# Kernel optimization log

Measured on AMD Instinct MI355X. Metric: run time of the kernel, lower is better.

Reference implementation:

```python
import jax, jax.numpy as jnp
import numpy as np

B, S, E, H, MLP = 2, 2048, 1024, 16, 4096
VEC = 8          # args.vec_length: block-row height of vector-sparse mask
SPARSITY = 0.9   # fraction of attention entries dropped
D = E // H


def _make_mask():
    # static_random_mask_aligned: each block-row of VEC query rows keeps a
    # random ~(1-sparsity) subset of key columns. Diagonal kept so every
    # softmax row is non-empty.
    rng = np.random.default_rng(0)
    block = rng.random((S // VEC, S)) < (1.0 - SPARSITY)   # [m, n]
    mask = np.repeat(block, VEC, axis=0)                   # [S, S]
    mask |= np.eye(S, dtype=bool)
    return jnp.asarray(mask)


def setup_inputs() -> dict:
    key = jax.random.key(0)
    ks = jax.random.split(key, 8)
    w = lambda k, shp: (0.02 * jax.random.normal(k, shp, dtype=jnp.float32))
    return {
        "x": jax.random.normal(ks[0], (B, S, E), dtype=jnp.float32),
        "mask": _make_mask(),                       # [S,S] bool, static
        "w_qkv": w(ks[1], (3 * E, E)),             # in_proj_weight
        "b_qkv": jnp.zeros((3 * E,), jnp.float32),
        "w_out": w(ks[2], (E, E)),                 # out_proj
        "b_out": jnp.zeros((E,), jnp.float32),
        "g1": jnp.ones((E,), jnp.float32), "beta1": jnp.zeros((E,), jnp.float32),
        "g2": jnp.ones((E,), jnp.float32), "beta2": jnp.zeros((E,), jnp.float32),
        "w1": w(ks[3], (MLP, E)), "bias1": jnp.zeros((MLP,), jnp.float32),
        "w2": w(ks[4], (E, MLP)), "bias2": jnp.zeros((E,), jnp.float32),
    }


def _layer_norm(x, g, b, eps=1e-5):
    mu = jnp.mean(x, axis=-1, keepdims=True)
    var = jnp.mean(jnp.square(x - mu), axis=-1, keepdims=True)
    return (x - mu) * jax.lax.rsqrt(var + eps) * g + b


def _sparse_mha(h, mask, w_qkv, b_qkv, w_out, b_out):
    qkv = jnp.einsum("bse,fe->bsf", h, w_qkv) + b_qkv       # [B,S,3E]
    q, k, v = jnp.split(qkv, 3, axis=-1)
    q = q.reshape(B, S, H, D)
    k = k.reshape(B, S, H, D)
    v = v.reshape(B, S, H, D)
    scores = jnp.einsum("bqhd,bkhd->bhqk", q, k) / jnp.sqrt(jnp.float32(D))
    scores = jnp.where(mask[None, None], scores, jnp.float32(-1e9))
    p = jax.nn.softmax(scores, axis=-1)
    ctx = jnp.einsum("bhqk,bkhd->bqhd", p, v).reshape(B, S, E)
    return jnp.einsum("bse,fe->bsf", ctx, w_out) + b_out


def reference(x, mask, w_qkv, b_qkv, w_out, b_out, g1, beta1, g2, beta2,
              w1, bias1, w2, bias2):
    h = _layer_norm(x, g1, beta1)
    attn = _sparse_mha(h, mask, w_qkv, b_qkv, w_out, b_out)
    out = attn + x                      # residual 1
    out = _layer_norm(out, g2, beta2)
    out = jnp.einsum("bse,me->bsm", out, w1) + bias1   # linear1 (no activation, as in source)
    out = jnp.einsum("bsm,em->bse", out, w2) + bias2   # linear2
    return out + x                      # residual adds ORIGINAL x (as in source)
```

## Files before the change

### kernel.cpp

```cpp
#include <hip/hip_runtime.h>
#include <cstdint>
#include <cstddef>

typedef unsigned short u16;
typedef unsigned int u32;
typedef short s16x8 __attribute__((ext_vector_type(8)));
typedef float f32x4 __attribute__((ext_vector_type(4)));
typedef _Float16 f16x2 __attribute__((ext_vector_type(2)));

__device__ __forceinline__ float fdot2(f16x2 a, f16x2 b, float c) {
#if defined(__HIP_DEVICE_COMPILE__) && __has_builtin(__builtin_amdgcn_fdot2)
  return __builtin_amdgcn_fdot2(a, b, c, false);
#else
  return (float)a.x * (float)b.x + (float)a.y * (float)b.y + c;
#endif
}

__device__ __forceinline__ float red8(float x) {
#if defined(__HIP_DEVICE_COMPILE__)
  asm("v_add_f32_dpp %0, %0, %0 quad_perm:[1,0,3,2] row_mask:0xf bank_mask:0xf"
      : "+v"(x));
  asm("v_add_f32_dpp %0, %0, %0 quad_perm:[2,3,0,1] row_mask:0xf bank_mask:0xf"
      : "+v"(x));
  asm("v_add_f32_dpp %0, %0, %0 row_half_mirror row_mask:0xf bank_mask:0xf"
      : "+v"(x));
  return x;
#else
  x += __shfl_xor(x, 1); x += __shfl_xor(x, 2); x += __shfl_xor(x, 4);
  return x;
#endif
}

__device__ __forceinline__ void fmamix_lo(float& a, u32 hv, float p) {
#if defined(__HIP_DEVICE_COMPILE__)
  asm("v_fma_mix_f32 %0, %1, %2, %0 op_sel_hi:[1,0,0]"
      : "+v"(a) : "v"(hv), "v"(p));
#else
  union { u32 i; _Float16 h[2]; } c; c.i = hv; a += (float)c.h[0] * p;
#endif
}
__device__ __forceinline__ void fmamix_hi(float& a, u32 hv, float p) {
#if defined(__HIP_DEVICE_COMPILE__)
  asm("v_fma_mix_f32 %0, %1, %2, %0 op_sel:[1,0,0] op_sel_hi:[1,0,0]"
      : "+v"(a) : "v"(hv), "v"(p));
#else
  union { u32 i; _Float16 h[2]; } c; c.i = hv; a += (float)c.h[1] * p;
#endif
}

#define S_LEN 2048
#define EMB   1024
#define NHEAD 16
#define HD    64
#define E3    3072
#define MLPD  4096
#define NROWS 4096
#define LCAP  640

__device__ __forceinline__ float bf2f(u16 v) {
  union { u32 i; float f; } c; c.i = ((u32)v) << 16; return c.f;
}
__device__ __forceinline__ u16 f2bf(float f) {
  union { float f; u32 i; } c; c.f = f;
  u32 x = c.i;
  return (u16)((x + 0x7FFFu + ((x >> 16) & 1u)) >> 16);
}
__device__ __forceinline__ u16 f2h(float f) {
  _Float16 h = (_Float16)f;
  union { _Float16 h; u16 b; } c; c.h = h; return c.b;
}

__device__ __forceinline__ void gl2lds16(const void* g, void* l) {
  __builtin_amdgcn_global_load_lds(
      (__attribute__((address_space(1))) void*)(g),
      (__attribute__((address_space(3))) void*)(l), 16, 0, 0);
}

__global__ void detect_flags(const u32* __restrict__ w1s, int* __restrict__ dtflag,
                             const u32* __restrict__ mask, int* __restrict__ maskrep) {
  __shared__ int hits[256];
  __shared__ u32 red[256];
  int h = 0; u32 v = 0;
  for (int i = threadIdx.x; i < 4096; i += 256) {
    u32 w = w1s[i];
    if ((w & 0xFFFFu) && (((w >> 7) & 0xFFu) >= 0xC8u)) ++h;
    v |= mask[i];
  }
  hits[threadIdx.x] = h; red[threadIdx.x] = v;
  __syncthreads();
  if (threadIdx.x == 0) {
    int t = 0; u32 o = 0;
    for (int i = 0; i < 256; ++i) { t += hits[i]; o |= red[i]; }
    *dtflag = (t > 8) ? 1 : 0;
    int rep;
    if (o <= 1u) rep = 0;
    else if (o & 0x80u) rep = 1;
    else if (o & 0x00800000u) rep = 2;
    else rep = 3;
    *maskrep = rep;
  }
}

__device__ __forceinline__ bool maskbit(const void* m, int rep, size_t idx) {
  switch (rep) {
    case 0:  return ((const int*)m)[idx] != 0;
    case 1:  return ((const u16*)m)[idx] != 0;
    case 2:  return ((const u32*)m)[idx] != 0;
    default: return ((const unsigned char*)m)[idx] != 0;
  }
}

__global__ __launch_bounds__(256)
void cvt_kernel(const void* __restrict__ src, u16* __restrict__ dst,
                int n8, const int* __restrict__ dtflag) {
  const int i = blockIdx.x * blockDim.x + threadIdx.x;
  if (i >= n8) return;
  if (*dtflag) {
    const float4 a = ((const float4*)src)[i * 2];
    const float4 b = ((const float4*)src)[i * 2 + 1];
    u16 o[8] = {f2bf(a.x), f2bf(a.y), f2bf(a.z), f2bf(a.w),
                f2bf(b.x), f2bf(b.y), f2bf(b.z), f2bf(b.w)};
    *(uint4*)(dst + (size_t)i * 8) = *(const uint4*)o;
  } else {
    ((uint4*)dst)[i] = ((const uint4*)src)[i];
  }
}

__global__ void cvt_small(const void* s0, u16* d0, const void* s1, u16* d1,
                          const void* s2, u16* d2, const void* s3, u16* d3,
                          const void* s4, u16* d4, const void* s5, u16* d5,
                          const void* s6, u16* d6, const void* s7, u16* d7,
                          const int* __restrict__ dtflag) {
  const int f = *dtflag;
  const void* srcs[8] = {s0, s1, s2, s3, s4, s5, s6, s7};
  u16* dsts[8] = {d0, d1, d2, d3, d4, d5, d6, d7};
  const int ns[8] = {E3, EMB, EMB, EMB, EMB, EMB, MLPD, EMB};
#pragma unroll
  for (int k = 0; k < 8; ++k) {
    for (int idx = threadIdx.x; idx < ns[k]; idx += 256)
      dsts[k][idx] = f ? f2bf(((const float*)srcs[k])[idx])
                       : ((const u16*)srcs[k])[idx];
  }
}

__global__ void build_lists(const void* __restrict__ mask, const int* __restrict__ repf,
                            int* __restrict__ lists, int* __restrict__ cnt,
                            unsigned char* __restrict__ diagflag) {
  __shared__ int num;
  const int m = blockIdx.x;
  if (threadIdx.x == 0) num = 0;
  __syncthreads();
  const int rep = *repf;
  const int row0 = m * 8;
  for (int j = threadIdx.x; j < S_LEN; j += 256) {
    int srcrow = (j == row0) ? (row0 + 1) : row0;
    bool bit = maskbit(mask, rep, (size_t)srcrow * S_LEN + j);
    if (j >= row0 && j < row0 + 8) diagflag[j] = bit ? 0 : 1;
    if (bit) {
      int p = atomicAdd(&num, 1);
      if (p < LCAP) lists[m * LCAP + p] = j * 4096;
    }
  }
  __syncthreads();
  if (threadIdx.x == 0) cnt[m] = (num < LCAP) ? num : LCAP;
}

__global__ __launch_bounds__(256)
void ln_kernel(const void* __restrict__ Xv, const u16* __restrict__ g,
               const u16* __restrict__ be, u16* __restrict__ O,
               const int* __restrict__ inf32) {
  const int wv = threadIdx.x >> 6, ln = threadIdx.x & 63;
  const int row = blockIdx.x * 4 + wv;
  float v[16];
  if (inf32 && *inf32) {
    const float* xr = (const float*)Xv + (size_t)row * EMB;
    float4 a0 = *(const float4*)(xr + ln * 8);
    float4 a1 = *(const float4*)(xr + ln * 8 + 4);
    float4 b0 = *(const float4*)(xr + 512 + ln * 8);
    float4 b1 = *(const float4*)(xr + 512 + ln * 8 + 4);
    v[0]=a0.x; v[1]=a0.y; v[2]=a0.z; v[3]=a0.w; v[4]=a1.x; v[5]=a1.y; v[6]=a1.z; v[7]=a1.w;
    v[8]=b0.x; v[9]=b0.y; v[10]=b0.z; v[11]=b0.w; v[12]=b1.x; v[13]=b1.y; v[14]=b1.z; v[15]=b1.w;
  } else {
    const u16* xr = (const u16*)Xv + (size_t)row * EMB;
    union { uint4 u; u16 s[8]; } p0, p1;
    p0.u = *(const uint4*)(xr + ln * 8);
    p1.u = *(const uint4*)(xr + 512 + ln * 8);
#pragma unroll
    for (int t = 0; t < 8; ++t) { v[t] = bf2f(p0.s[t]); v[8 + t] = bf2f(p1.s[t]); }
  }
  float s = 0.f, sq = 0.f;
#pragma unroll
  for (int t = 0; t < 16; ++t) { s += v[t]; sq += v[t] * v[t]; }
#pragma unroll
  for (int off = 32; off; off >>= 1) { s += __shfl_xor(s, off); sq += __shfl_xor(sq, off); }
  const float mu = s * (1.0f / EMB);
  const float var = sq * (1.0f / EMB) - mu * mu;
  const float rsig = rsqrtf(var + 1e-5f);
  union { uint4 u; u16 s[8]; } g0, g1v, b0, b1v, o0, o1;
  g0.u = *(const uint4*)(g + ln * 8);   g1v.u = *(const uint4*)(g + 512 + ln * 8);
  b0.u = *(const uint4*)(be + ln * 8);  b1v.u = *(const uint4*)(be + 512 + ln * 8);
#pragma unroll
  for (int t = 0; t < 8; ++t) {
    o0.s[t] = f2bf((v[t]     - mu) * rsig * bf2f(g0.s[t])  + bf2f(b0.s[t]));
    o1.s[t] = f2bf((v[8 + t] - mu) * rsig * bf2f(g1v.s[t]) + bf2f(b1v.s[t]));
  }
  u16* orow = O + (size_t)row * EMB;
  *(uint4*)(orow + ln * 8) = o0.u;
  *(uint4*)(orow + 512 + ln * 8) = o1.u;
}

__global__ __launch_bounds__(256)
void gemm_bt(const u16* __restrict__ A, const u16* __restrict__ B,
             const u16* __restrict__ bias, u16* __restrict__ C,
             int M, int N, int K) {
  __shared__ u16 a_sh[128 * 64];
  __shared__ u16 b_sh[128 * 64];
  const int tid = threadIdx.x;
  const int wv = tid >> 6, ln = tid & 63;
  const int wm = wv & 1, wn = wv >> 1;
  const int tm = blockIdx.y, tn = blockIdx.x;
  const int srow = ln >> 3;
  const int scol = ((ln & 7) ^ srow) * 8;
  const int q = ln >> 4, rr = ln & 15;

  f32x4 acc[4][4] = {};
  const u16* Abase = A + (size_t)(tm * 128) * K;
  const u16* Bbase = B + (size_t)(tn * 128) * K;

  for (int k0 = 0; k0 < K; k0 += 64) {
    __syncthreads();
#pragma unroll
    for (int c = 0; c < 4; ++c) {
      const int chunk = wv * 4 + c;
      const int row = chunk * 8 + srow;
      gl2lds16(Abase + (size_t)row * K + k0 + scol, &a_sh[chunk * 512]);
      gl2lds16(Bbase + (size_t)row * K + k0 + scol, &b_sh[chunk * 512]);
    }
    __syncthreads();
#pragma unroll
    for (int kk = 0; kk < 2; ++kk) {
      const int slot = ((kk * 4 + q) ^ (rr & 7)) * 8;
      s16x8 af[4], bfr[4];
#pragma unroll
      for (int mi = 0; mi < 4; ++mi)
        af[mi] = *(const s16x8*)&a_sh[(wm * 64 + mi * 16 + rr) * 64 + slot];
#pragma unroll
      for (int ni = 0; ni < 4; ++ni)
        bfr[ni] = *(const s16x8*)&b_sh[(wn * 64 + ni * 16 + rr) * 64 + slot];
#pragma unroll
      for (int mi = 0; mi < 4; ++mi)
#pragma unroll
        for (int ni = 0; ni < 4; ++ni)
          acc[mi][ni] = __builtin_amdgcn_mfma_f32_16x16x32_bf16(af[mi], bfr[ni], acc[mi][ni], 0, 0, 0);
    }
  }
#pragma unroll
  for (int ni = 0; ni < 4; ++ni) {
    const int col = tn * 128 + wn * 64 + ni * 16 + rr;
    const float bv = bf2f(bias[col]);
#pragma unroll
    for (int mi = 0; mi < 4; ++mi)
#pragma unroll
      for (int r2 = 0; r2 < 4; ++r2) {
        const int row = tm * 128 + wm * 64 + mi * 16 + q * 4 + r2;
        C[(size_t)row * N + col] = f2bf(acc[mi][ni][r2] + bv);
      }
  }
}

__global__ __launch_bounds__(256)
void gemm_bt_sk(const u16* __restrict__ A, const u16* __restrict__ B,
                u16* __restrict__ P0, u16* __restrict__ P1,
                int M, int N, int K) {
  __shared__ u16 a_sh[128 * 64];
  __shared__ u16 b_sh[128 * 64];
  const int tid = threadIdx.x;
  const int wv = tid >> 6, ln = tid & 63;
  const int wm = wv & 1, wn = wv >> 1;
  const int tm = blockIdx.y, tn = blockIdx.x, kz = blockIdx.z;
  const int Kh = K >> 1;
  const int koff = kz * Kh;
  const int srow = ln >> 3;
  const int scol = ((ln & 7) ^ srow) * 8;
  const int q = ln >> 4, rr = ln & 15;

  f32x4 acc[4][4] = {};
  const u16* Abase = A + (size_t)(tm * 128) * K + koff;
  const u16* Bbase = B + (size_t)(tn * 128) * K + koff;

  for (int k0 = 0; k0 < Kh; k0 += 64) {
    __syncthreads();
#pragma unroll
    for (int c = 0; c < 4; ++c) {
      const int chunk = wv * 4 + c;
      const int row = chunk * 8 + srow;
      gl2lds16(Abase + (size_t)row * K + k0 + scol, &a_sh[chunk * 512]);
      gl2lds16(Bbase + (size_t)row * K + k0 + scol, &b_sh[chunk * 512]);
    }
    __syncthreads();
#pragma unroll
    for (int kk = 0; kk < 2; ++kk) {
      const int slot = ((kk * 4 + q) ^ (rr & 7)) * 8;
      s16x8 af[4], bfr[4];
#pragma unroll
      for (int mi = 0; mi < 4; ++mi)
        af[mi] = *(const s16x8*)&a_sh[(wm * 64 + mi * 16 + rr) * 64 + slot];
#pragma unroll
      for (int ni = 0; ni < 4; ++ni)
        bfr[ni] = *(const s16x8*)&b_sh[(wn * 64 + ni * 16 + rr) * 64 + slot];
#pragma unroll
      for (int mi = 0; mi < 4; ++mi)
#pragma unroll
        for (int ni = 0; ni < 4; ++ni)
          acc[mi][ni] = __builtin_amdgcn_mfma_f32_16x16x32_bf16(af[mi], bfr[ni], acc[mi][ni], 0, 0, 0);
    }
  }
  u16* P = kz ? P1 : P0;
#pragma unroll
  for (int ni = 0; ni < 4; ++ni) {
    const int col = tn * 128 + wn * 64 + ni * 16 + rr;
#pragma unroll
    for (int mi = 0; mi < 4; ++mi)
#pragma unroll
      for (int r2 = 0; r2 < 4; ++r2) {
        const int row = tm * 128 + wm * 64 + mi * 16 + q * 4 + r2;
        P[(size_t)row * N + col] = f2bf(acc[mi][ni][r2]);
      }
  }
}

__global__ __launch_bounds__(256)
void combine_kernel(const u16* __restrict__ P0, const u16* __restrict__ P1,
                    const u16* __restrict__ bias, const void* __restrict__ xr,
                    void* __restrict__ Ov, const int* __restrict__ f32io) {
  const int i = blockIdx.x * 256 + threadIdx.x;
  const int col8 = (i & 127) * 8;
  union { uint4 u; u16 s[8]; } a, b, bi;
  a.u = ((const uint4*)P0)[i];
  b.u = ((const uint4*)P1)[i];
  bi.u = *(const uint4*)(bias + col8);
  const int f = *f32io;
  float o[8];
#pragma unroll
  for (int t = 0; t < 8; ++t) o[t] = bf2f(a.s[t]) + bf2f(b.s[t]) + bf2f(bi.s[t]);
  if (f) {
    const float4 x0 = ((const float4*)xr)[i * 2];
    const float4 x1 = ((const float4*)xr)[i * 2 + 1];
    o[0]+=x0.x; o[1]+=x0.y; o[2]+=x0.z; o[3]+=x0.w;
    o[4]+=x1.x; o[5]+=x1.y; o[6]+=x1.z; o[7]+=x1.w;
    float4 r0 = {o[0],o[1],o[2],o[3]}, r1 = {o[4],o[5],o[6],o[7]};
    ((float4*)Ov)[i * 2] = r0;
    ((float4*)Ov)[i * 2 + 1] = r1;
  } else {
    union { uint4 u; u16 s[8]; } xv;
    xv.u = ((const uint4*)xr)[i];
    u16 r[8];
#pragma unroll
    for (int t = 0; t < 8; ++t) r[t] = f2bf(o[t] + bf2f(xv.s[t]));
    ((uint4*)Ov)[i] = *(const uint4*)r;
  }
}

__global__ __launch_bounds__(256)
void gemm_qkv(const u16* __restrict__ A, const u16* __restrict__ B,
              const u16* __restrict__ bias,
              u16* __restrict__ Qb, u16* __restrict__ KVp,
              int K) {
  __shared__ u16 a_sh[128 * 64];
  __shared__ u16 b_sh[128 * 64];
  const int tid = threadIdx.x;
  const int wv = tid >> 6, ln = tid & 63;
  const int wm = wv & 1, wn = wv >> 1;
  const int tm = blockIdx.y, tn = blockIdx.x;
  const int srow = ln >> 3;
  const int scol = ((ln & 7) ^ srow) * 8;
  const int q = ln >> 4, rr = ln & 15;

  f32x4 acc[4][4] = {};
  const u16* Abase = A + (size_t)(tm * 128) * K;
  const u16* Bbase = B + (size_t)(tn * 128) * K;

  for (int k0 = 0; k0 < K; k0 += 64) {
    __syncthreads();
#pragma unroll
    for (int c = 0; c < 4; ++c) {
      const int chunk = wv * 4 + c;
      const int row = chunk * 8 + srow;
      gl2lds16(Abase + (size_t)row * K + k0 + scol, &a_sh[chunk * 512]);
      gl2lds16(Bbase + (size_t)row * K + k0 + scol, &b_sh[chunk * 512]);
    }
    __syncthreads();
#pragma unroll
    for (int kk = 0; kk < 2; ++kk) {
      const int slot = ((kk * 4 + q) ^ (rr & 7)) * 8;
      s16x8 af[4], bfr[4];
#pragma unroll
      for (int mi = 0; mi < 4; ++mi)
        af[mi] = *(const s16x8*)&a_sh[(wm * 64 + mi * 16 + rr) * 64 + slot];
#pragma unroll
      for (int ni = 0; ni < 4; ++ni)
        bfr[ni] = *(const s16x8*)&b_sh[(wn * 64 + ni * 16 + rr) * 64 + slot];
#pragma unroll
      for (int mi = 0; mi < 4; ++mi)
#pragma unroll
        for (int ni = 0; ni < 4; ++ni)
          acc[mi][ni] = __builtin_amdgcn_mfma_f32_16x16x32_bf16(af[mi], bfr[ni], acc[mi][ni], 0, 0, 0);
    }
  }
  const int third = (tn * 128) >> 10;
#pragma unroll
  for (int ni = 0; ni < 4; ++ni) {
    const int col = tn * 128 + wn * 64 + ni * 16 + rr;
    const int w = col & 1023;
    const float bv = bf2f(bias[col]);
#pragma unroll
    for (int mi = 0; mi < 4; ++mi)
#pragma unroll
      for (int r2 = 0; r2 < 4; ++r2) {
        const int row = tm * 128 + wm * 64 + mi * 16 + q * 4 + r2;
        const float o = acc[mi][ni][r2] + bv;
        if (third == 0) {
          Qb[(size_t)row * 1024 + w] = f2bf(o);
        } else {
          const int hh = w >> 6, d = w & 63;
          KVp[(size_t)row * 2048 + hh * 128 + ((third == 1) ? 0 : 64) + d] = f2h(o);
        }
      }
  }
}

__global__ __launch_bounds__(256)
void gemm_bt_n64(const u16* __restrict__ A, const u16* __restrict__ B,
                 const u16* __restrict__ bias, const void* __restrict__ resid,
                 void* __restrict__ Cv, int M, int N, int K,
                 const int* __restrict__ residf32, const int* __restrict__ outf32) {
  __shared__ u16 a_sh[128 * 64];
  __shared__ u16 b_sh[64 * 64];
  const int tid = threadIdx.x;
  const int wv = tid >> 6, ln = tid & 63;
  const int wm = wv & 1, wn = wv >> 1;
  const int tm = blockIdx.y, tn = blockIdx.x;
  const int srow = ln >> 3;
  const int scol = ((ln & 7) ^ srow) * 8;
  const int q = ln >> 4, rr = ln & 15;

  f32x4 acc[4][2] = {};
  const u16* Abase = A + (size_t)(tm * 128) * K;
  const u16* Bbase = B + (size_t)(tn * 64) * K;

  for (int k0 = 0; k0 < K; k0 += 64) {
    __syncthreads();
#pragma unroll
    for (int c = 0; c < 4; ++c) {
      const int chunk = wv * 4 + c;
      const int row = chunk * 8 + srow;
      gl2lds16(Abase + (size_t)row * K + k0 + scol, &a_sh[chunk * 512]);
    }
#pragma unroll
    for (int c = 0; c < 2; ++c) {
      const int chunk = wv * 2 + c;
      const int row = chunk * 8 + srow;
      gl2lds16(Bbase + (size_t)row * K + k0 + scol, &b_sh[chunk * 512]);
    }
    __syncthreads();
#pragma unroll
    for (int kk = 0; kk < 2; ++kk) {
      const int slot = ((kk * 4 + q) ^ (rr & 7)) * 8;
      s16x8 af[4], bfr[2];
#pragma unroll
      for (int mi = 0; mi < 4; ++mi)
        af[mi] = *(const s16x8*)&a_sh[(wm * 64 + mi * 16 + rr) * 64 + slot];
#pragma unroll
      for (int ni = 0; ni < 2; ++ni)
        bfr[ni] = *(const s16x8*)&b_sh[(wn * 32 + ni * 16 + rr) * 64 + slot];
#pragma unroll
      for (int mi = 0; mi < 4; ++mi)
#pragma unroll
        for (int ni = 0; ni < 2; ++ni)
          acc[mi][ni] = __builtin_amdgcn_mfma_f32_16x16x32_bf16(af[mi], bfr[ni], acc[mi][ni], 0, 0, 0);
    }
  }
  const int rf32 = residf32 ? *residf32 : 0;
  const int f32o = outf32 ? *outf32 : 0;
#pragma unroll
  for (int ni = 0; ni < 2; ++ni) {
    const int col = tn * 64 + wn * 32 + ni * 16 + rr;
    const float bv = bf2f(bias[col]);
#pragma unroll
    for (int mi = 0; mi < 4; ++mi)
#pragma unroll
      for (int r2 = 0; r2 < 4; ++r2) {
        const int row = tm * 128 + wm * 64 + mi * 16 + q * 4 + r2;
        const size_t idx = (size_t)row * N + col;
        float o = acc[mi][ni][r2] + bv;
        if (resid)
          o += rf32 ? ((const float*)resid)[idx] : bf2f(((const u16*)resid)[idx]);
        if (f32o) ((float*)Cv)[idx] = o;
        else      ((u16*)Cv)[idx] = f2bf(o);
      }
  }
}

__global__ __launch_bounds__(512)
void attn_kernel(const u16* __restrict__ Qb, const u16* __restrict__ KVp,
                 const int* __restrict__ lists,
                 const int* __restrict__ cnt, const unsigned char* __restrict__ diagflag,
                 u16* __restrict__ ctx) {
  __shared__ int list_sh[LCAP];
  const int g = blockIdx.x;
  const int b = g >> 12;
  const int h = (g >> 8) & 15;
  const int m = g & 255;
  const int tid = threadIdx.x, wv = tid >> 6, ln = tid & 63;
  const int es = ln >> 3, dc = ln & 7;
  const int i = m * 8 + wv;
  const int n = cnt[m];

  for (int e = tid; e < n; e += 512) list_sh[e] = lists[m * LCAP + e];
  __syncthreads();

  const u16* qrow = Qb + (size_t)(b * S_LEN + i) * EMB + h * 64 + dc * 8;
  union { uint4 u; u16 s[8]; } qi; qi.u = *(const uint4*)qrow;
  f16x2 q2[4];
  const float qs = 0.125f * 1.44269504f;
#pragma unroll
  for (int t = 0; t < 4; ++t) {
    q2[t].x = (_Float16)(bf2f(qi.s[2 * t])     * qs);
    q2[t].y = (_Float16)(bf2f(qi.s[2 * t + 1]) * qs);
  }

  const char* kvb = (const char*)KVp + (size_t)b * S_LEN * 4096;
  const u32 loff = (u32)(h * 256 + dc * 16);

  float sum = 0.f;
  float acc[8] = {};

  auto score = [&](const uint4& ku) -> float {
    union { uint4 u; f16x2 p[4]; } kk; kk.u = ku;
    float s = fdot2(kk.p[3], q2[3], fdot2(kk.p[2], q2[2],
              fdot2(kk.p[1], q2[1], fdot2(kk.p[0], q2[0], 0.f))));
    s = red8(s);
    s = fminf(fmaxf(s, -126.f), 126.f);
    return exp2f(s);
  };
  auto doV = [&](const uint4& vu, float p) {
    fmamix_lo(acc[0], vu.x, p); fmamix_hi(acc[1], vu.x, p);
    fmamix_lo(acc[2], vu.y, p); fmamix_hi(acc[3], vu.y, p);
    fmamix_lo(acc[4], vu.z, p); fmamix_hi(acc[5], vu.z, p);
    fmamix_lo(acc[6], vu.w, p); fmamix_hi(acc[7], vu.w, p);
  };

  const int df = diagflag[i];
  if (df) {
    const u32 dioff = (u32)(i * 4096) + loff;
    const uint4 ku = *(const uint4*)(kvb + dioff);
    const uint4 vu = *(const uint4*)(kvb + dioff + 128);
    float p = score(ku);
    p = (es == 0) ? p : 0.f;
    sum += p;
    doV(vu, p);
  }

  int e0 = 0;
  for (; e0 + 32 <= n; e0 += 32) {
    const u32 oA = (u32)list_sh[e0 + es] + loff;
    const u32 oB = (u32)list_sh[e0 + 8 + es] + loff;
    const u32 oC = (u32)list_sh[e0 + 16 + es] + loff;
    const u32 oD = (u32)list_sh[e0 + 24 + es] + loff;
    const uint4 kA = *(const uint4*)(kvb + oA);
    const uint4 kB = *(const uint4*)(kvb + oB);
    const uint4 kC = *(const uint4*)(kvb + oC);
    const uint4 kD = *(const uint4*)(kvb + oD);
    const uint4 vA = *(const uint4*)(kvb + oA + 128);
    const uint4 vB = *(const uint4*)(kvb + oB + 128);
    const uint4 vC = *(const uint4*)(kvb + oC + 128);
    const uint4 vD = *(const uint4*)(kvb + oD + 128);
    const float pA = score(kA);
    const float pB = score(kB);
    const float pC = score(kC);
    const float pD = score(kD);
    sum += (pA + pB) + (pC + pD);
    doV(vA, pA);
    doV(vB, pB);
    doV(vC, pC);
    doV(vD, pD);
  }
  for (; e0 + 8 <= n; e0 += 8) {
    const u32 off = (u32)list_sh[e0 + es] + loff;
    const uint4 ku = *(const uint4*)(kvb + off);
    const uint4 vu = *(const uint4*)(kvb + off + 128);
    const float p = score(ku);
    sum += p;
    doV(vu, p);
  }
  if (e0 < n) {
    const int e = e0 + es;
    const bool valid = (e < n);
    const u32 off = (u32)(valid ? list_sh[e] : list_sh[0]) + loff;
    const uint4 ku = *(const uint4*)(kvb + off);
    const uint4 vu = *(const uint4*)(kvb + off + 128);
    float p = score(ku);
    p = valid ? p : 0.f;
    sum += p;
    doV(vu, p);
  }

#pragma unroll
  for (int off = 8; off < 64; off <<= 1) {
    sum += __shfl_xor(sum, off);
#pragma unroll
    for (int t = 0; t < 8; ++t) acc[t] += __shfl_xor(acc[t], off);
  }

  if (es == 0) {
    const float inv = 1.0f / sum;
    u16 o[8];
#pragma unroll
    for (int t = 0; t < 8; ++t) o[t] = f2bf(acc[t] * inv);
    *(uint4*)(ctx + (size_t)(b * S_LEN + i) * EMB + h * 64 + dc * 8) = *(const uint4*)o;
  }
}

extern "C" void kernel_launch(void* const* d_in, const int* in_sizes, int n_in,
                              void* d_out, int out_size, void* d_ws, size_t ws_size,
                              hipStream_t stream) {
  const void* x_raw    = d_in[0];
  const void* mask     = d_in[1];
  const void* wqkv_raw = d_in[2];
  const void* bqkv_raw = d_in[3];
  const void* wout_raw = d_in[4];
  const void* bout_raw = d_in[5];
  const void* g1_raw   = d_in[6];
  const void* be1_raw  = d_in[7];
  const void* g2_raw   = d_in[8];
  const void* be2_raw  = d_in[9];
  const void* w1_raw   = d_in[10];
  const void* b1_raw   = d_in[11];
  const void* w2_raw   = d_in[12];
  const void* b2_raw   = d_in[13];

  char* ws = (char*)d_ws;
  const size_t MB = 1u << 20;
  int* dtflag         = (int*)ws;
  int* maskrep        = (int*)(ws + 64);
  int* cnt            = (int*)(ws + 1024);
  unsigned char* dfl  = (unsigned char*)(ws + 4096);
  int* lists          = (int*)(ws + 8192);
  u16* R1  = (u16*)(ws + 1 * MB);
  u16* Qb  = (u16*)(ws + 9 * MB);
  u16* KVp = (u16*)(ws + 17 * MB);
  u16* M1  = (u16*)(ws + 17 * MB);
  u16* W   = (u16*)(ws + 49 * MB);
  char* sm = ws + 57 * MB;
  u16* bq  = (u16*)(sm);
  u16* bo  = (u16*)(sm + 8192);
  u16* g1b = (u16*)(sm + 16384);
  u16* be1b= (u16*)(sm + 24576);
  u16* g2b = (u16*)(sm + 32768);
  u16* be2b= (u16*)(sm + 40960);
  u16* b1b = (u16*)(sm + 49152);
  u16* b2b = (u16*)(sm + 65536);

  detect_flags<<<dim3(1), dim3(256), 0, stream>>>((const u32*)w1_raw, dtflag,
                                                  (const u32*)mask, maskrep);
  build_lists<<<dim3(256), dim3(256), 0, stream>>>(mask, maskrep, lists, cnt, dfl);
  cvt_small<<<dim3(1), dim3(256), 0, stream>>>(
      bqkv_raw, bq, bout_raw, bo, g1_raw, g1b, be1_raw, be1b,
      g2_raw, g2b, be2_raw, be2b, b1_raw, b1b, b2_raw, b2b, dtflag);

  auto cvt = [&](const void* src, u16* dst, int n) {
    const int n8 = n / 8;
    cvt_kernel<<<dim3((n8 + 255) / 256), dim3(256), 0, stream>>>(src, dst, n8, dtflag);
  };

  ln_kernel<<<dim3(NROWS / 4), dim3(256), 0, stream>>>(x_raw, g1b, be1b, R1, dtflag);
  cvt(wqkv_raw, W, E3 * EMB);
  gemm_qkv<<<dim3(E3 / 128, NROWS / 128), dim3(256), 0, stream>>>(
      R1, W, bq, Qb, KVp, EMB);
  attn_kernel<<<dim3(2 * NHEAD * 256), dim3(512), 0, stream>>>(
      Qb, KVp, lists, cnt, dfl, R1);
  cvt(wout_raw, W, EMB * EMB);
  gemm_bt_n64<<<dim3(EMB / 64, NROWS / 128), dim3(256), 0, stream>>>(
      R1, W, bo, x_raw, Qb, NROWS, EMB, EMB, dtflag, nullptr);
  ln_kernel<<<dim3(NROWS / 4), dim3(256), 0, stream>>>(Qb, g2b, be2b, R1, nullptr);
  cvt(w1_raw, W, MLPD * EMB);
  gemm_bt<<<dim3(MLPD / 128, NROWS / 128), dim3(256), 0, stream>>>(
      R1, W, b1b, M1, NROWS, MLPD, EMB);
  cvt(w2_raw, W, EMB * MLPD);
  gemm_bt_sk<<<dim3(EMB / 128, NROWS / 128, 2), dim3(256), 0, stream>>>(
      M1, W, R1, Qb, NROWS, EMB, MLPD);
  combine_kernel<<<dim3(NROWS * EMB / 8 / 256), dim3(256), 0, stream>>>(
      R1, Qb, b2b, x_raw, d_out, dtflag);
}
```

Baseline: 469.2 us.

## Process four query rows per wave in sparse attention to reuse K/V loads

```diff
diff --git a/kernel.cpp b/kernel.cpp
--- a/kernel.cpp
+++ b/kernel.cpp
@@ -501,7 +501,7 @@
   }
 }
 
-__global__ __launch_bounds__(512)
+__global__ __launch_bounds__(128)
 void attn_kernel(const u16* __restrict__ Qb, const u16* __restrict__ KVp,
                  const int* __restrict__ lists,
                  const int* __restrict__ cnt, const unsigned char* __restrict__ diagflag,
@@ -513,111 +513,140 @@
   const int m = g & 255;
   const int tid = threadIdx.x, wv = tid >> 6, ln = tid & 63;
   const int es = ln >> 3, dc = ln & 7;
-  const int i = m * 8 + wv;
+  const int i0 = m * 8 + wv * 4;
   const int n = cnt[m];
 
-  for (int e = tid; e < n; e += 512) list_sh[e] = lists[m * LCAP + e];
+  for (int e = tid; e < n; e += 128) list_sh[e] = lists[m * LCAP + e];
   __syncthreads();
 
-  const u16* qrow = Qb + (size_t)(b * S_LEN + i) * EMB + h * 64 + dc * 8;
-  union { uint4 u; u16 s[8]; } qi; qi.u = *(const uint4*)qrow;
-  f16x2 q2[4];
   const float qs = 0.125f * 1.44269504f;
-#pragma unroll
-  for (int t = 0; t < 4; ++t) {
-    q2[t].x = (_Float16)(bf2f(qi.s[2 * t])     * qs);
-    q2[t].y = (_Float16)(bf2f(qi.s[2 * t + 1]) * qs);
+  f16x2 q[4][4];
+#pragma unroll
+  for (int r = 0; r < 4; ++r) {
+    const u16* qrow = Qb + (size_t)(b * S_LEN + i0 + r) * EMB + h * 64 + dc * 8;
+    union { uint4 u; u16 s[8]; } qi; qi.u = *(const uint4*)qrow;
+#pragma unroll
+    for (int t = 0; t < 4; ++t) {
+      q[r][t].x = (_Float16)(bf2f(qi.s[2 * t])     * qs);
+      q[r][t].y = (_Float16)(bf2f(qi.s[2 * t + 1]) * qs);
+    }
   }
 
   const char* kvb = (const char*)KVp + (size_t)b * S_LEN * 4096;
   const u32 loff = (u32)(h * 256 + dc * 16);
 
-  float sum = 0.f;
-  float acc[8] = {};
-
-  auto score = [&](const uint4& ku) -> float {
-    union { uint4 u; f16x2 p[4]; } kk; kk.u = ku;
-    float s = fdot2(kk.p[3], q2[3], fdot2(kk.p[2], q2[2],
-              fdot2(kk.p[1], q2[1], fdot2(kk.p[0], q2[0], 0.f))));
+  float sum[4] = {};
+  float acc[4][8] = {};
+
+  auto score1 = [&](const uint4& ku, int r) -> float {
+    union { uint4 u; f16x2 kk[4]; } K; K.u = ku;
+    float s = 0.f;
+    if (r == 0) s = fdot2(K.kk[3], q[0][3], fdot2(K.kk[2], q[0][2],
+                   fdot2(K.kk[1], q[0][1], fdot2(K.kk[0], q[0][0], 0.f))));
+    else if (r == 1) s = fdot2(K.kk[3], q[1][3], fdot2(K.kk[2], q[1][2],
+                   fdot2(K.kk[1], q[1][1], fdot2(K.kk[0], q[1][0], 0.f))));
+    else if (r == 2) s = fdot2(K.kk[3], q[2][3], fdot2(K.kk[2], q[2][2],
+                   fdot2(K.kk[1], q[2][1], fdot2(K.kk[0], q[2][0], 0.f))));
+    else s = fdot2(K.kk[3], q[3][3], fdot2(K.kk[2], q[3][2],
+                   fdot2(K.kk[1], q[3][1], fdot2(K.kk[0], q[3][0], 0.f))));
     s = red8(s);
     s = fminf(fmaxf(s, -126.f), 126.f);
     return exp2f(s);
   };
-  auto doV = [&](const uint4& vu, float p) {
-    fmamix_lo(acc[0], vu.x, p); fmamix_hi(acc[1], vu.x, p);
-    fmamix_lo(acc[2], vu.y, p); fmamix_hi(acc[3], vu.y, p);
-    fmamix_lo(acc[4], vu.z, p); fmamix_hi(acc[5], vu.z, p);
-    fmamix_lo(acc[6], vu.w, p); fmamix_hi(acc[7], vu.w, p);
+
+  auto PROC = [&](const uint4& ku, const uint4& vu) {
+#pragma unroll
+    for (int r = 0; r < 4; ++r) {
+      const float p = score1(ku, r);
+      sum[r] += p;
+      fmamix_lo(acc[r][0], vu.x, p); fmamix_hi(acc[r][1], vu.x, p);
+      fmamix_lo(acc[r][2], vu.y, p); fmamix_hi(acc[r][3], vu.y, p);
+      fmamix_lo(acc[r][4], vu.z, p); fmamix_hi(acc[r][5], vu.z, p);
+      fmamix_lo(acc[r][6], vu.w, p); fmamix_hi(acc[r][7], vu.w, p);
+    }
   };
 
-  const int df = diagflag[i];
-  if (df) {
-    const u32 dioff = (u32)(i * 4096) + loff;
-    const uint4 ku = *(const uint4*)(kvb + dioff);
-    const uint4 vu = *(const uint4*)(kvb + dioff + 128);
-    float p = score(ku);
-    p = (es == 0) ? p : 0.f;
-    sum += p;
-    doV(vu, p);
+#pragma unroll
+  for (int r = 0; r < 4; ++r) {
+    if (diagflag[i0 + r]) {
+      const u32 off = (u32)((i0 + r) * 4096) + loff;
+      const uint4 ku = *(const uint4*)(kvb + off);
+      const uint4 vu = *(const uint4*)(kvb + off + 128);
+      float p = score1(ku, r);
+      p = (es == 0) ? p : 0.f;
+      sum[r] += p;
+      fmamix_lo(acc[r][0], vu.x, p); fmamix_hi(acc[r][1], vu.x, p);
+      fmamix_lo(acc[r][2], vu.y, p); fmamix_hi(acc[r][3], vu.y, p);
+      fmamix_lo(acc[r][4], vu.z, p); fmamix_hi(acc[r][5], vu.z, p);
+      fmamix_lo(acc[r][6], vu.w, p); fmamix_hi(acc[r][7], vu.w, p);
+    }
   }
 
   int e0 = 0;
-  for (; e0 + 32 <= n; e0 += 32) {
-    const u32 oA = (u32)list_sh[e0 + es] + loff;
-    const u32 oB = (u32)list_sh[e0 + 8 + es] + loff;
-    const u32 oC = (u32)list_sh[e0 + 16 + es] + loff;
-    const u32 oD = (u32)list_sh[e0 + 24 + es] + loff;
-    const uint4 kA = *(const uint4*)(kvb + oA);
-    const uint4 kB = *(const uint4*)(kvb + oB);
-    const uint4 kC = *(const uint4*)(kvb + oC);
-    const uint4 kD = *(const uint4*)(kvb + oD);
-    const uint4 vA = *(const uint4*)(kvb + oA + 128);
-    const uint4 vB = *(const uint4*)(kvb + oB + 128);
-    const uint4 vC = *(const uint4*)(kvb + oC + 128);
-    const uint4 vD = *(const uint4*)(kvb + oD + 128);
-    const float pA = score(kA);
-    const float pB = score(kB);
-    const float pC = score(kC);
-    const float pD = score(kD);
-    sum += (pA + pB) + (pC + pD);
-    doV(vA, pA);
-    doV(vB, pB);
-    doV(vC, pC);
-    doV(vD, pD);
+  if (n >= 16) {
+    uint4 k0, v0, k1, v1;
+    {
+      const u32 o0 = (u32)list_sh[es] + loff;
+      const u32 o1 = (u32)list_sh[8 + es] + loff;
+      k0 = *(const uint4*)(kvb + o0); v0 = *(const uint4*)(kvb + o0 + 128);
+      k1 = *(const uint4*)(kvb + o1); v1 = *(const uint4*)(kvb + o1 + 128);
+    }
+    for (; e0 + 32 <= n; e0 += 16) {
+      const u32 o0 = (u32)list_sh[e0 + 16 + es] + loff;
+      const u32 o1 = (u32)list_sh[e0 + 24 + es] + loff;
+      const uint4 nk0 = *(const uint4*)(kvb + o0), nv0 = *(const uint4*)(kvb + o0 + 128);
+      const uint4 nk1 = *(const uint4*)(kvb + o1), nv1 = *(const uint4*)(kvb + o1 + 128);
+      PROC(k0, v0);
+      PROC(k1, v1);
+      k0 = nk0; v0 = nv0; k1 = nk1; v1 = nv1;
+    }
+    PROC(k0, v0);
+    PROC(k1, v1);
+    e0 += 16;
   }
   for (; e0 + 8 <= n; e0 += 8) {
-    const u32 off = (u32)list_sh[e0 + es] + loff;
-    const uint4 ku = *(const uint4*)(kvb + off);
-    const uint4 vu = *(const uint4*)(kvb + off + 128);
-    const float p = score(ku);
-    sum += p;
-    doV(vu, p);
+    const u32 o = (u32)list_sh[e0 + es] + loff;
+    const uint4 ku = *(const uint4*)(kvb + o);
+    const uint4 vu = *(const uint4*)(kvb + o + 128);
+    PROC(ku, vu);
   }
   if (e0 < n) {
     const int e = e0 + es;
     const bool valid = (e < n);
-    const u32 off = (u32)(valid ? list_sh[e] : list_sh[0]) + loff;
-    const uint4 ku = *(const uint4*)(kvb + off);
-    const uint4 vu = *(const uint4*)(kvb + off + 128);
-    float p = score(ku);
-    p = valid ? p : 0.f;
-    sum += p;
-    doV(vu, p);
+    const u32 o = (u32)(valid ? list_sh[e] : list_sh[0]) + loff;
+    const uint4 ku = *(const uint4*)(kvb + o);
+    const uint4 vu = *(const uint4*)(kvb + o + 128);
+#pragma unroll
+    for (int r = 0; r < 4; ++r) {
+      float p = score1(ku, r);
+      p = valid ? p : 0.f;
+      sum[r] += p;
+      fmamix_lo(acc[r][0], vu.x, p); fmamix_hi(acc[r][1], vu.x, p);
+      fmamix_lo(acc[r][2], vu.y, p); fmamix_hi(acc[r][3], vu.y, p);
+      fmamix_lo(acc[r][4], vu.z, p); fmamix_hi(acc[r][5], vu.z, p);
+      fmamix_lo(acc[r][6], vu.w, p); fmamix_hi(acc[r][7], vu.w, p);
+    }
   }
 
 #pragma unroll
   for (int off = 8; off < 64; off <<= 1) {
-    sum += __shfl_xor(sum, off);
-#pragma unroll
-    for (int t = 0; t < 8; ++t) acc[t] += __shfl_xor(acc[t], off);
+#pragma unroll
+    for (int r = 0; r < 4; ++r) {
+      sum[r] += __shfl_xor(sum[r], off);
+#pragma unroll
+      for (int t = 0; t < 8; ++t) acc[r][t] += __shfl_xor(acc[r][t], off);
+    }
   }
 
   if (es == 0) {
-    const float inv = 1.0f / sum;
-    u16 o[8];
-#pragma unroll
-    for (int t = 0; t < 8; ++t) o[t] = f2bf(acc[t] * inv);
-    *(uint4*)(ctx + (size_t)(b * S_LEN + i) * EMB + h * 64 + dc * 8) = *(const uint4*)o;
+#pragma unroll
+    for (int r = 0; r < 4; ++r) {
+      const float inv = 1.0f / sum[r];
+      u16 o[8];
+#pragma unroll
+      for (int t = 0; t < 8; ++t) o[t] = f2bf(acc[r][t] * inv);
+      *(uint4*)(ctx + (size_t)(b * S_LEN + i0 + r) * EMB + h * 64 + dc * 8) = *(const uint4*)o;
+    }
   }
 }
 
@@ -677,7 +706,7 @@
   cvt(wqkv_raw, W, E3 * EMB);
   gemm_qkv<<<dim3(E3 / 128, NROWS / 128), dim3(256), 0, stream>>>(
       R1, W, bq, Qb, KVp, EMB);
-  attn_kernel<<<dim3(2 * NHEAD * 256), dim3(512), 0, stream>>>(
+  attn_kernel<<<dim3(2 * NHEAD * 256), dim3(128), 0, stream>>>(
       Qb, KVp, lists, cnt, dfl, R1);
   cvt(wout_raw, W, EMB * EMB);
   gemm_bt_n64<<<dim3(EMB / 64, NROWS / 128), dim3(256), 0, stream>>>(
```

New measurement: 430.1 us. -8.3%, faster.
